# Performance work log

Measured on AMD Instinct MI355X. Metric: run time of the kernel, lower is better.

The kernel has to match this reference:

```python
import jax, jax.numpy as jnp
import numpy as np

B, T, P, V, D, DINO, H, L = 32, 40, 256, 4096, 256, 384, 4, 2
HD = D // H          # head dim 64
DFF = 4 * D          # 1024
EPS = 1e-5


def setup_inputs() -> dict:
    key = jax.random.key(0)
    ks = iter(jax.random.split(key, 40))
    rn = lambda shape, s=0.02: jax.random.normal(next(ks), shape, jnp.float32) * s
    return dict(
        patches=jax.random.normal(next(ks), (B, P, DINO), jnp.float32),
        tokens=jax.random.randint(next(ks), (B, T), 0, V, jnp.int32),
        tok_emb=rn((V, D)),
        pos_emb=rn((1, T, D)),
        qkv_w=rn((L, 3 * D, D)), qkv_b=jnp.zeros((L, 3 * D), jnp.float32),
        out_w=rn((L, D, D)), out_b=jnp.zeros((L, D), jnp.float32),
        ln1_s=jnp.ones((L, D), jnp.float32), ln1_b=jnp.zeros((L, D), jnp.float32),
        w1=rn((L, DFF, D)), b1=jnp.zeros((L, DFF), jnp.float32),
        w2=rn((L, D, DFF)), b2=jnp.zeros((L, D), jnp.float32),
        ln2_s=jnp.ones((L, D), jnp.float32), ln2_b=jnp.zeros((L, D), jnp.float32),
        fus_w1=rn((D, DINO + D)), fus_b1=jnp.zeros((D,), jnp.float32),
        fus_w2=rn((D, D)), fus_b2=jnp.zeros((D,), jnp.float32),
        cls_w=rn((V, D)), cls_b=jnp.zeros((V,), jnp.float32),
    )


def _ln(x, s, b):
    m = jnp.mean(x, -1, keepdims=True)
    v = jnp.var(x, -1, keepdims=True)
    return (x - m) * jax.lax.rsqrt(v + EPS) * s + b


def _token_encoder(tokens, tok_emb, pos_emb, qkv_w, qkv_b, out_w, out_b,
                   ln1_s, ln1_b, w1, b1, w2, b2, ln2_s, ln2_b):
    # Causal full-sequence pass: output at position t equals re-running the
    # unmasked encoder on tokens[:, :t+1] and taking the last position.
    x = tok_emb[tokens] + pos_emb[:, :tokens.shape[1], :]   # [B,T,D]
    causal = jnp.triu(jnp.full((T, T), -1e9, jnp.float32), 1)  # [T,T]
    for l in range(L):  # fixed small layer count
        qkv = x @ qkv_w[l].T + qkv_b[l]                     # [B,T,3D]
        q, k, v = jnp.split(qkv, 3, axis=-1)
        q = q.reshape(B, T, H, HD).transpose(0, 2, 1, 3)    # [B,H,T,hd]
        k = k.reshape(B, T, H, HD).transpose(0, 2, 1, 3)
        v = v.reshape(B, T, H, HD).transpose(0, 2, 1, 3)
        scores = jnp.einsum('bhqd,bhkd->bhqk', q, k) / np.sqrt(HD).astype(np.float32)
        attn = jax.nn.softmax(scores + causal, axis=-1)
        ctx = jnp.einsum('bhqk,bhkd->bhqd', attn, v)        # [B,H,T,hd]
        ctx = ctx.transpose(0, 2, 1, 3).reshape(B, T, D)
        x = _ln(x + ctx @ out_w[l].T + out_b[l], ln1_s[l], ln1_b[l])
        h = jax.nn.relu(x @ w1[l].T + b1[l]) @ w2[l].T + b2[l]
        x = _ln(x + h, ln2_s[l], ln2_b[l])
    return x  # [B,T,D]


def reference(patches, tokens, tok_emb, pos_emb, qkv_w, qkv_b, out_w, out_b,
              ln1_s, ln1_b, w1, b1, w2, b2, ln2_s, ln2_b,
              fus_w1, fus_b1, fus_w2, fus_b2, cls_w, cls_b):
    enc = _token_encoder(tokens, tok_emb, pos_emb, qkv_w, qkv_b, out_w, out_b,
                         ln1_s, ln1_b, w1, b1, w2, b2, ln2_s, ln2_b)  # [B,T,D]
    # context for step 0 is zeros; step t>0 uses encoder output at position t-1
    ctx = jnp.concatenate([jnp.zeros((B, 1, D), enc.dtype), enc[:, :-1]], axis=1)  # [B,T,D]
    # fusion MLP: split the concat-linear into a patch part and a context part
    wp, wc = fus_w1[:, :DINO], fus_w1[:, DINO:]
    pproj = patches @ wp.T                                  # [B,P,D]
    cproj = ctx @ wc.T + fus_b1                             # [B,T,D]
    h = jax.nn.gelu(pproj[:, None, :, :] + cproj[:, :, None, :], approximate=False)  # [B,T,P,D]
    fused = h @ fus_w2.T + fus_b2                           # [B,T,P,D]
    # sigmoid+gather of the 4096-way logits == gather classifier rows, dot, sigmoid
    w_sel = cls_w[tokens]                                   # [B,T,D]
    b_sel = cls_b[tokens]                                   # [B,T]
    logits = jnp.einsum('btpd,btd->btp', fused, w_sel) + b_sel[:, :, None]
    probs = jax.nn.sigmoid(logits)                          # [B,T,P]
    return probs.transpose(0, 2, 1)                         # [B,P,T] == [B,256,40]
```

## Files before the change

kernel.cpp:

```cpp
#include <hip/hip_runtime.h>
#include <hip/hip_bf16.h>

#define B_ 32
#define T_ 40
#define P_ 256
#define V_ 4096
#define D_ 256
#define DINO_ 384
#define H_ 4
#define L_ 2
#define HD_ 64
#define DFF_ 1024
#define EPS_ 1e-5f

typedef __bf16 bf16;
typedef __bf16 bf16x8 __attribute__((ext_vector_type(8)));
typedef float f32x4 __attribute__((ext_vector_type(4)));

#define FUS_ELEMS 163840
#define FUS_BLOCKS 80
#define PAT_BLOCKS 1536
#define PREP_UNITS 2960

__device__ __forceinline__ bf16x8 cvt8(const float* p) {
  float4 f0 = *(const float4*)p;
  float4 f1 = *(const float4*)(p + 4);
  bf16x8 v;
  v[0] = (bf16)f0.x; v[1] = (bf16)f0.y; v[2] = (bf16)f0.z; v[3] = (bf16)f0.w;
  v[4] = (bf16)f1.x; v[5] = (bf16)f1.y; v[6] = (bf16)f1.z; v[7] = (bf16)f1.w;
  return v;
}

struct GemmSM  { bf16 As[32 * 72];  bf16 Ws[32 * 72]; };
struct CprojSM { bf16 As[32 * 264]; bf16 Ws[32 * 72]; };
struct AttnSM  { float q[20][65]; float k[40][65]; float v[40][65]; float s[20][41]; };
struct PrepSM  { float tile[32][33]; };
struct FinalSM { float2 cws[4][D_]; };

struct Params {
  const float* patches; const int* tokens; const float* tok_emb; const float* pos_emb;
  const float* qkv_w; const float* qkv_b; const float* out_w; const float* out_b;
  const float* ln1_s; const float* ln1_b; const float* w1; const float* b1;
  const float* w2; const float* b2; const float* ln2_s; const float* ln2_b;
  const float* fus_w1; const float* fus_b1; const float* fus_w2; const float* fus_b2;
  const float* cls_w; const float* cls_b; float* out;
  float* x; float* qkvbuf; float* attbuf; float* s; float* pprojT; float* cw;
  bf16* wb; bf16* w2Tb; bf16* patb; bf16* hb;
};

template <int ABF16, int WF32, int OBF16, int RELU, int RESID, int GATH, int CW>
__device__ __forceinline__ void tile_gemm(
    bf16* As, bf16* Ws, const void* Av, const void* Wv, const float* bias,
    const float* resid, const int* tokens, void* outv, int K, int lda,
    int ldw, int ldc, int bm, int bn) {
  const int tid = threadIdx.x;
  const int lane = tid & 63;
  const int wv = tid >> 6;
  const int mi = wv & 1, ni = wv >> 1;
  const int col = lane & 15, quad = lane >> 4;
  const int srow = tid >> 3, kc = (tid & 7) * 8;
  const float* Af = (const float*)Av;
  const bf16* Ab = (const bf16*)Av;
  const float* Ag = GATH ? (Af + (long)tokens[bm + srow] * D_) : nullptr;
  const float* Wpf = (const float*)Wv + (long)(bn + srow) * ldw + kc;
  const bf16* Wpb = (const bf16*)Wv + (long)(bn + srow) * ldw + kc;

  f32x4 acc = {0.f, 0.f, 0.f, 0.f};
  for (int kk = 0; kk < K; kk += 64) {
    if (GATH)
      *(bf16x8*)&As[srow * 72 + kc] = cvt8(Ag + kk + kc);
    else if (ABF16)
      *(bf16x8*)&As[srow * 72 + kc] = *(const bf16x8*)(Ab + (long)(bm + srow) * lda + kk + kc);
    else
      *(bf16x8*)&As[srow * 72 + kc] = cvt8(Af + (long)(bm + srow) * lda + kk + kc);
    if (WF32)
      *(bf16x8*)&Ws[srow * 72 + kc] = cvt8(Wpf + kk);
    else
      *(bf16x8*)&Ws[srow * 72 + kc] = *(const bf16x8*)(Wpb + kk);
    __syncthreads();
#pragma unroll
    for (int ki = 0; ki < 2; ++ki) {
      bf16x8 afr = *(const bf16x8*)&As[(mi * 16 + col) * 72 + ki * 32 + quad * 8];
      bf16x8 bfr = *(const bf16x8*)&Ws[(ni * 16 + col) * 72 + ki * 32 + quad * 8];
      acc = __builtin_amdgcn_mfma_f32_16x16x32_bf16(afr, bfr, acc, 0, 0, 0);
    }
    __syncthreads();
  }
  const int n = bn + ni * 16 + col;
  float bv = bias ? bias[n] : 0.0f;
#pragma unroll
  for (int r = 0; r < 4; ++r) {
    int m = bm + mi * 16 + quad * 4 + r;
    float val = acc[r] + bv;
    if (RESID) val += resid[(long)m * D_ + n];
    if (RELU) val = fmaxf(val, 0.0f);
    if (CW == 1) ((float*)outv)[(long)m * (2 * D_) + n * 2] = val;
    else if (CW == 2) ((float*)outv)[(long)m * (2 * D_) + n * 2 + 1] = val;
    else if (OBF16) ((bf16*)outv)[(long)m * ldc + n] = (bf16)val;
    else ((float*)outv)[(long)m * ldc + n] = val;
  }
}

__device__ __forceinline__ void do_prep(PrepSM& ps, const Params& P, int u) {
  int tid = threadIdx.x;
  if (u < 1280) {
    P.x[u * D_ + tid] = P.tok_emb[(long)P.tokens[u] * D_ + tid] + P.pos_emb[(u % T_) * D_ + tid];
  } else if (u < 1344) {
    int tt = u - 1280;
    int bx = (tt & 7) * 32, by = (tt >> 3) * 32;
    int tx = tid & 31, ty = tid >> 5;
#pragma unroll
    for (int i = 0; i < 32; i += 8) ps.tile[ty + i][tx] = P.fus_w2[(by + ty + i) * D_ + bx + tx];
    __syncthreads();
#pragma unroll
    for (int i = 0; i < 32; i += 8)
      P.w2Tb[(bx + ty + i) * D_ + by + tx] = (bf16)ps.tile[tx][ty + i];
  } else if (u < 1344 + FUS_BLOCKS) {
    long f = (long)(u - 1344) * 2048 + tid * 8;
    *(bf16x8*)&P.wb[f] = cvt8(P.fus_w1 + f);
  } else {
    long f = (long)(u - 1344 - FUS_BLOCKS) * 2048 + tid * 8;
    *(bf16x8*)&P.patb[f] = cvt8(P.patches + f);
  }
}

__device__ __forceinline__ void do_qkv(GemmSM& g, const Params& P, int l, int u) {
  tile_gemm<0, 1, 0, 0, 0, 0, 0>(g.As, g.Ws, P.x, P.qkv_w + (long)l * 3 * D_ * D_,
                                 P.qkv_b + l * 3 * D_, nullptr, nullptr, P.qkvbuf,
                                 256, D_, D_, 3 * D_, (u / 24) * 32, (u % 24) * 32);
}
__device__ __forceinline__ void do_proj(GemmSM& g, const Params& P, int l, int u) {
  tile_gemm<0, 1, 0, 0, 1, 0, 0>(g.As, g.Ws, P.attbuf, P.out_w + (long)l * D_ * D_,
                                 P.out_b + l * D_, P.x, nullptr, P.s,
                                 256, D_, D_, D_, (u / 8) * 32, (u % 8) * 32);
}
__device__ __forceinline__ void do_w1(GemmSM& g, const Params& P, int l, int u) {
  tile_gemm<0, 1, 1, 1, 0, 0, 0>(g.As, g.Ws, P.x, P.w1 + (long)l * DFF_ * D_,
                                 P.b1 + l * DFF_, nullptr, nullptr, P.hb,
                                 256, D_, D_, DFF_, (u / 32) * 32, (u % 32) * 32);
}
__device__ __forceinline__ void do_w2(GemmSM& g, const Params& P, int l, int u) {
  tile_gemm<1, 1, 0, 0, 1, 0, 0>(g.As, g.Ws, P.hb, P.w2 + (long)l * D_ * DFF_,
                                 P.b2 + l * D_, P.x, nullptr, P.s,
                                 DFF_, DFF_, DFF_, D_, (u / 8) * 32, (u % 8) * 32);
}
__device__ __forceinline__ void do_pproj(GemmSM& g, const Params& P, int t) {
  int bn = (t & 7) * 32; int y = t >> 3; int bb = y >> 3; int bm = (y & 7) * 32;
  tile_gemm<1, 0, 0, 0, 0, 0, 0>(g.As, g.Ws, P.wb, P.patb + (long)bb * P_ * DINO_,
                                 nullptr, nullptr, nullptr, P.pprojT + (long)bb * D_ * P_,
                                 384, 640, DINO_, P_, bm, bn);
}
__device__ __forceinline__ void do_weff(GemmSM& g, const Params& P, int t) {
  tile_gemm<0, 0, 0, 0, 0, 1, 2>(g.As, g.Ws, P.cls_w, P.w2Tb, nullptr, nullptr,
                                 P.tokens, P.cw, 256, D_, D_, D_,
                                 (t / 8) * 32, (t % 8) * 32);
}

__device__ __forceinline__ void do_attn(AttnSM& A, const Params& P, int u) {
  int h = u & 3, b = (u >> 2) & 31, zq = u >> 7;
  int r0 = zq * 20;
  int tid = threadIdx.x;
  int lane = tid & 63, wv = tid >> 6;
  const float* qkv = P.qkvbuf;
  for (int idx = tid; idx < T_ * HD_; idx += 256) {
    int t = idx >> 6, d = idx & 63;
    long base = (long)(b * T_ + t) * (3 * D_) + h * HD_ + d;
    A.k[t][d] = qkv[base + D_];
    A.v[t][d] = qkv[base + 2 * D_];
    if (t < 20) A.q[t][d] = qkv[(long)(b * T_ + r0 + t) * (3 * D_) + h * HD_ + d];
  }
  __syncthreads();
  for (int idx = tid; idx < 20 * T_; idx += 256) {
    int i = idx / T_, j = idx - i * T_;
    if (j <= r0 + i) {
      float acc = 0.f;
#pragma unroll
      for (int d = 0; d < HD_; ++d) acc += A.q[i][d] * A.k[j][d];
      A.s[i][j] = acc * 0.125f;
    }
  }
  __syncthreads();
  for (int rr = wv; rr < 20; rr += 4) {
    int hi = r0 + rr;
    float val = (lane <= hi) ? A.s[rr][lane] : -1e30f;
    float mx = val;
#pragma unroll
    for (int mk = 1; mk < 64; mk <<= 1) mx = fmaxf(mx, __shfl_xor(mx, mk));
    float e = (lane <= hi)
                  ? __builtin_amdgcn_exp2f((val - mx) * 1.4426950408889634f)
                  : 0.f;
    float sum = e;
#pragma unroll
    for (int mk = 1; mk < 64; mk <<= 1) sum += __shfl_xor(sum, mk);
    float inv = __builtin_amdgcn_rcpf(sum);
    if (lane < T_) A.s[rr][lane] = e * inv;
  }
  __syncthreads();
  for (int idx = tid; idx < 20 * HD_; idx += 256) {
    int i = idx >> 6, d = idx & 63;
    int hi = r0 + i;
    float acc = 0.f;
    for (int j = 0; j <= hi; ++j) acc += A.s[i][j] * A.v[j][d];
    P.attbuf[(long)(b * T_ + hi) * D_ + h * HD_ + d] = acc;
  }
}

__device__ __forceinline__ void do_cproj(CprojSM& c, const Params& P, int bm, int bn) {
  const int tid = threadIdx.x;
  const int lane = tid & 63;
  const int wv = tid >> 6;
  const int mi = wv & 1, ni = wv >> 1;
  const int col = lane & 15, quad = lane >> 4;
  const int srow = tid >> 3, kc = (tid & 7) * 8;
  const int gm = bm + srow;
  f32x4 acc = {0.f, 0.f, 0.f, 0.f};
  const int cg = (tid & 7) * 32;
  const int t = gm % T_;
  if (t == 0) {
    bf16x8 z8 = {};
#pragma unroll
    for (int i = 0; i < 4; ++i) *(bf16x8*)&c.As[srow * 264 + cg + i * 8] = z8;
  } else {
    const float* sp = P.s + (long)(gm - 1) * D_ + cg;
    float v[32];
    float sum = 0.f, ss = 0.f;
#pragma unroll
    for (int i = 0; i < 8; ++i) {
      float4 f = *(const float4*)(sp + i * 4);
      v[i*4] = f.x; v[i*4+1] = f.y; v[i*4+2] = f.z; v[i*4+3] = f.w;
      sum += f.x + f.y + f.z + f.w;
      ss += f.x*f.x + f.y*f.y + f.z*f.z + f.w*f.w;
    }
#pragma unroll
    for (int mk = 1; mk < 8; mk <<= 1) {
      sum += __shfl_xor(sum, mk);
      ss += __shfl_xor(ss, mk);
    }
    float mean = sum * (1.0f / D_);
    float inv = rsqrtf(ss * (1.0f / D_) - mean * mean + EPS_);
    const float* lng = P.ln2_s + D_;
    const float* lnb = P.ln2_b + D_;
#pragma unroll
    for (int i = 0; i < 8; ++i) {
      float4 g4 = *(const float4*)(lng + cg + i * 4);
      float4 b4 = *(const float4*)(lnb + cg + i * 4);
      c.As[srow*264 + cg + i*4]     = (bf16)((v[i*4]   - mean) * inv * g4.x + b4.x);
      c.As[srow*264 + cg + i*4 + 1] = (bf16)((v[i*4+1] - mean) * inv * g4.y + b4.y);
      c.As[srow*264 + cg + i*4 + 2] = (bf16)((v[i*4+2] - mean) * inv * g4.z + b4.z);
      c.As[srow*264 + cg + i*4 + 3] = (bf16)((v[i*4+3] - mean) * inv * g4.w + b4.w);
    }
  }
  __syncthreads();
  const bf16* Wp = P.wb + 384 + (long)(bn + srow) * 640 + kc;
  for (int kk = 0; kk < 256; kk += 64) {
    *(bf16x8*)&c.Ws[srow * 72 + kc] = *(const bf16x8*)(Wp + kk);
    __syncthreads();
#pragma unroll
    for (int ki = 0; ki < 2; ++ki) {
      bf16x8 afr = *(const bf16x8*)&c.As[(mi*16 + col) * 264 + kk + ki*32 + quad*8];
      bf16x8 bfr = *(const bf16x8*)&c.Ws[(ni*16 + col) * 72 + ki*32 + quad*8];
      acc = __builtin_amdgcn_mfma_f32_16x16x32_bf16(afr, bfr, acc, 0, 0, 0);
    }
    __syncthreads();
  }
  const int n = bn + ni * 16 + col;
  float bv = P.fus_b1[n];
#pragma unroll
  for (int r = 0; r < 4; ++r) {
    int m = bm + mi * 16 + quad * 4 + r;
    P.cw[(long)m * (2 * D_) + n * 2] = acc[r] + bv;
  }
}

__device__ __forceinline__ void do_final(FinalSM& F, const Params& P, int u) {
  int tid = threadIdx.x;
  int lane = tid & 63, wv = tid >> 6;
  int px = u & 3, rest = u >> 2;
  int ty = rest % 10, b = rest / 10;
  int p = px * 64 + lane;
  int t = ty * 4 + wv;
  int mbase = b * T_ + ty * 4;
  for (int idx = tid; idx < 4 * D_; idx += 256) {
    int tt = idx >> 8, e = idx & 255;
    F.cws[tt][e] = ((const float2*)P.cw)[(long)(mbase + tt) * D_ + e];
  }
  __syncthreads();

  int m = b * T_ + t;
  int tok = P.tokens[m];
  const float* cr = P.cls_w + (long)tok * D_;
  float bacc = 0.f;
#pragma unroll
  for (int i = 0; i < 4; ++i) bacc += cr[lane + i * 64] * P.fus_b2[lane + i * 64];
#pragma unroll
  for (int mk = 1; mk < 64; mk <<= 1) bacc += __shfl_xor(bacc, mk);
  float beff = bacc + P.cls_b[tok];

  const float* ppb = P.pprojT + (long)b * (D_ * P_);
  float acc = 0.f;
#pragma unroll 8
  for (int e = 0; e < D_; ++e) {
    float pp = ppb[e * P_ + p];
    float2 c = F.cws[wv][e];
    float x = pp + c.x;
    float ex = __builtin_amdgcn_exp2f(-2.4554248f * x);
    float r = __builtin_amdgcn_rcpf(1.0f + ex);
    acc = fmaf(x * r, c.y, acc);
  }
  float logit = acc + beff;
  float es = __builtin_amdgcn_exp2f(-1.4426950408889634f * logit);
  P.out[(long)(b * P_ + p) * T_ + t] = __builtin_amdgcn_rcpf(1.0f + es);
}

__global__ __launch_bounds__(256) void prep_k(Params P) {
  __shared__ PrepSM ps; do_prep(ps, P, blockIdx.x);
}
__global__ __launch_bounds__(256) void qkv_k(Params P, int l) {
  __shared__ GemmSM g; do_qkv(g, P, l, blockIdx.x);
}
__global__ __launch_bounds__(256) void apw_k(Params P) {
  __shared__ union __align__(16) { AttnSM a; GemmSM g; } sm;
  int bid = blockIdx.x;
  if (bid < 256) do_attn(sm.a, P, bid);
  else if (bid < 2304) do_pproj(sm.g, P, bid - 256);
  else do_weff(sm.g, P, bid - 2304);
}
__global__ __launch_bounds__(256) void attn_k(Params P) {
  __shared__ AttnSM a; do_attn(a, P, blockIdx.x);
}
__global__ __launch_bounds__(256) void proj_k(Params P, int l) {
  __shared__ GemmSM g; do_proj(g, P, l, blockIdx.x);
}
__global__ __launch_bounds__(256) void ln_k(const float* __restrict__ s,
                                            float* __restrict__ xout,
                                            const float* __restrict__ g,
                                            const float* __restrict__ be) {
  int wv = threadIdx.x >> 6, lane = threadIdx.x & 63;
  int m = blockIdx.x * 4 + wv;
  float4 v = *(const float4*)(s + (long)m * D_ + lane * 4);
  float sum = v.x + v.y + v.z + v.w;
  float ss = v.x * v.x + v.y * v.y + v.z * v.z + v.w * v.w;
#pragma unroll
  for (int mk = 1; mk < 64; mk <<= 1) {
    sum += __shfl_xor(sum, mk);
    ss += __shfl_xor(ss, mk);
  }
  float mean = sum * (1.0f / D_);
  float inv = rsqrtf(ss * (1.0f / D_) - mean * mean + EPS_);
  float4 g4 = *(const float4*)(g + lane * 4);
  float4 b4 = *(const float4*)(be + lane * 4);
  float4 o;
  o.x = (v.x - mean) * inv * g4.x + b4.x;
  o.y = (v.y - mean) * inv * g4.y + b4.y;
  o.z = (v.z - mean) * inv * g4.z + b4.z;
  o.w = (v.w - mean) * inv * g4.w + b4.w;
  *(float4*)(xout + (long)m * D_ + lane * 4) = o;
}
__global__ __launch_bounds__(256) void w1_k(Params P, int l) {
  __shared__ GemmSM g; do_w1(g, P, l, blockIdx.x);
}
__global__ __launch_bounds__(256) void w2_k(Params P, int l) {
  __shared__ GemmSM g; do_w2(g, P, l, blockIdx.x);
}
__global__ __launch_bounds__(256) void cproj_k(Params P) {
  __shared__ CprojSM c; do_cproj(c, P, (blockIdx.x >> 3) * 32, (blockIdx.x & 7) * 32);
}
__global__ __launch_bounds__(256) void final_k(Params P) {
  __shared__ FinalSM f; do_final(f, P, blockIdx.x);
}

extern "C" void kernel_launch(void* const* d_in, const int* in_sizes, int n_in, void* d_out,
                              int out_size, void* d_ws, size_t ws_size, hipStream_t stream) {
  Params P;
  P.patches = (const float*)d_in[0];
  P.tokens = (const int*)d_in[1];
  P.tok_emb = (const float*)d_in[2];
  P.pos_emb = (const float*)d_in[3];
  P.qkv_w = (const float*)d_in[4];
  P.qkv_b = (const float*)d_in[5];
  P.out_w = (const float*)d_in[6];
  P.out_b = (const float*)d_in[7];
  P.ln1_s = (const float*)d_in[8];
  P.ln1_b = (const float*)d_in[9];
  P.w1 = (const float*)d_in[10];
  P.b1 = (const float*)d_in[11];
  P.w2 = (const float*)d_in[12];
  P.b2 = (const float*)d_in[13];
  P.ln2_s = (const float*)d_in[14];
  P.ln2_b = (const float*)d_in[15];
  P.fus_w1 = (const float*)d_in[16];
  P.fus_b1 = (const float*)d_in[17];
  P.fus_w2 = (const float*)d_in[18];
  P.fus_b2 = (const float*)d_in[19];
  P.cls_w = (const float*)d_in[20];
  P.cls_b = (const float*)d_in[21];
  P.out = (float*)d_out;

  const int MT = B_ * T_;
  P.x = (float*)d_ws;
  P.qkvbuf = P.x + MT * D_;
  P.attbuf = P.qkvbuf + MT * 3 * D_;
  P.s = P.attbuf + MT * D_;
  P.pprojT = P.s + MT * D_;
  P.cw = P.pprojT + (long)B_ * D_ * P_;
  P.wb = (bf16*)(P.cw + MT * D_ * 2);
  P.w2Tb = P.wb + FUS_ELEMS;
  P.patb = P.w2Tb + D_ * D_;
  P.hb = P.patb + (long)B_ * P_ * DINO_;

  prep_k<<<PREP_UNITS, 256, 0, stream>>>(P);
  qkv_k<<<960, 256, 0, stream>>>(P, 0);
  apw_k<<<2624, 256, 0, stream>>>(P);
  proj_k<<<320, 256, 0, stream>>>(P, 0);
  ln_k<<<320, 256, 0, stream>>>(P.s, P.x, P.ln1_s, P.ln1_b);
  w1_k<<<1280, 256, 0, stream>>>(P, 0);
  w2_k<<<320, 256, 0, stream>>>(P, 0);
  ln_k<<<320, 256, 0, stream>>>(P.s, P.x, P.ln2_s, P.ln2_b);
  qkv_k<<<960, 256, 0, stream>>>(P, 1);
  attn_k<<<256, 256, 0, stream>>>(P);
  proj_k<<<320, 256, 0, stream>>>(P, 1);
  ln_k<<<320, 256, 0, stream>>>(P.s, P.x, P.ln1_s + D_, P.ln1_b + D_);
  w1_k<<<1280, 256, 0, stream>>>(P, 1);
  w2_k<<<320, 256, 0, stream>>>(P, 1);
  cproj_k<<<320, 256, 0, stream>>>(P);
  final_k<<<1280, 256, 0, stream>>>(P);
}
```

Before: 249.6 us.

## Spread patch-projection and weff tiles across small encoder kernels; coarsen prep blocks

The 2048 independent patch-projection tiles, previously packed into one large kernel with attention, are split into four chunks of 512. Those chunks now ride along with the under-filled layer-0 QKV, attention, W2 and layer-1 QKV launches, and the weff work moves into the layer-0 output-projection launch. The intent is to fill idle compute units during the small encoder GEMMs and shorten the critical path. The prep kernel also gets coarser blocks: float4 embedding rows, four rows per block, and four conversion chunks per block. This cuts the launch from 2960 blocks to 788. The risk is load imbalance, since the heavier pproj tiles can now extend those kernels.

Measured after the change: 249.0 us. Within noise of the previous version (-0.2%).

```diff
diff --git a/kernel.cpp b/kernel.cpp
--- a/kernel.cpp
+++ b/kernel.cpp
@@ -18,9 +18,9 @@
 typedef float f32x4 __attribute__((ext_vector_type(4)));
 
 #define FUS_ELEMS 163840
-#define FUS_BLOCKS 80
-#define PAT_BLOCKS 1536
-#define PREP_UNITS 2960
+#define FUS_BLOCKS 20
+#define PAT_BLOCKS 384
+#define PREP_UNITS 788
 
 __device__ __forceinline__ bf16x8 cvt8(const float* p) {
   float4 f0 = *(const float4*)p;
@@ -103,10 +103,17 @@
 
 __device__ __forceinline__ void do_prep(PrepSM& ps, const Params& P, int u) {
   int tid = threadIdx.x;
-  if (u < 1280) {
-    P.x[u * D_ + tid] = P.tok_emb[(long)P.tokens[u] * D_ + tid] + P.pos_emb[(u % T_) * D_ + tid];
-  } else if (u < 1344) {
-    int tt = u - 1280;
+  if (u < 320) {
+    int r = tid >> 6, lane = tid & 63;
+    int m = u * 4 + r;
+    long eb = (long)P.tokens[m] * D_ + lane * 4;
+    long pb = (long)(m % T_) * D_ + lane * 4;
+    float4 e = *(const float4*)(P.tok_emb + eb);
+    float4 p = *(const float4*)(P.pos_emb + pb);
+    float4 o; o.x = e.x + p.x; o.y = e.y + p.y; o.z = e.z + p.z; o.w = e.w + p.w;
+    *(float4*)(P.x + (long)m * D_ + lane * 4) = o;
+  } else if (u < 384) {
+    int tt = u - 320;
     int bx = (tt & 7) * 32, by = (tt >> 3) * 32;
     int tx = tid & 31, ty = tid >> 5;
 #pragma unroll
@@ -115,12 +122,20 @@
 #pragma unroll
     for (int i = 0; i < 32; i += 8)
       P.w2Tb[(bx + ty + i) * D_ + by + tx] = (bf16)ps.tile[tx][ty + i];
-  } else if (u < 1344 + FUS_BLOCKS) {
-    long f = (long)(u - 1344) * 2048 + tid * 8;
-    *(bf16x8*)&P.wb[f] = cvt8(P.fus_w1 + f);
+  } else if (u < 384 + FUS_BLOCKS) {
+    long base = (long)(u - 384) * 8192;
+#pragma unroll
+    for (int j = 0; j < 4; ++j) {
+      long f = base + j * 2048 + tid * 8;
+      *(bf16x8*)&P.wb[f] = cvt8(P.fus_w1 + f);
+    }
   } else {
-    long f = (long)(u - 1344 - FUS_BLOCKS) * 2048 + tid * 8;
-    *(bf16x8*)&P.patb[f] = cvt8(P.patches + f);
+    long base = (long)(u - 384 - FUS_BLOCKS) * 8192;
+#pragma unroll
+    for (int j = 0; j < 4; ++j) {
+      long f = base + j * 2048 + tid * 8;
+      *(bf16x8*)&P.patb[f] = cvt8(P.patches + f);
+    }
   }
 }
 
@@ -315,18 +330,27 @@
 __global__ __launch_bounds__(256) void prep_k(Params P) {
   __shared__ PrepSM ps; do_prep(ps, P, blockIdx.x);
 }
-__global__ __launch_bounds__(256) void qkv_k(Params P, int l) {
-  __shared__ GemmSM g; do_qkv(g, P, l, blockIdx.x);
-}
-__global__ __launch_bounds__(256) void apw_k(Params P) {
+template <int L, int CH>
+__global__ __launch_bounds__(256) void qkvp_k(Params P) {
+  __shared__ GemmSM g;
+  int bid = blockIdx.x;
+  if (bid < 960) do_qkv(g, P, L, bid);
+  else do_pproj(g, P, bid - 960 + CH * 512);
+}
+__global__ __launch_bounds__(256) void attnp_k(Params P) {
   __shared__ union __align__(16) { AttnSM a; GemmSM g; } sm;
   int bid = blockIdx.x;
   if (bid < 256) do_attn(sm.a, P, bid);
-  else if (bid < 2304) do_pproj(sm.g, P, bid - 256);
-  else do_weff(sm.g, P, bid - 2304);
+  else do_pproj(sm.g, P, bid - 256 + 512);
 }
 __global__ __launch_bounds__(256) void attn_k(Params P) {
   __shared__ AttnSM a; do_attn(a, P, blockIdx.x);
+}
+__global__ __launch_bounds__(256) void projw_k(Params P) {
+  __shared__ GemmSM g;
+  int bid = blockIdx.x;
+  if (bid < 320) do_proj(g, P, 0, bid);
+  else do_weff(g, P, bid - 320);
 }
 __global__ __launch_bounds__(256) void proj_k(Params P, int l) {
   __shared__ GemmSM g; do_proj(g, P, l, blockIdx.x);
@@ -358,6 +382,12 @@
 }
 __global__ __launch_bounds__(256) void w1_k(Params P, int l) {
   __shared__ GemmSM g; do_w1(g, P, l, blockIdx.x);
+}
+__global__ __launch_bounds__(256) void w2p_k(Params P) {
+  __shared__ GemmSM g;
+  int bid = blockIdx.x;
+  if (bid < 320) do_w2(g, P, 0, bid);
+  else do_pproj(g, P, bid - 320 + 1024);
 }
 __global__ __launch_bounds__(256) void w2_k(Params P, int l) {
   __shared__ GemmSM g; do_w2(g, P, l, blockIdx.x);
@@ -409,14 +439,14 @@
   P.hb = P.patb + (long)B_ * P_ * DINO_;
 
   prep_k<<<PREP_UNITS, 256, 0, stream>>>(P);
-  qkv_k<<<960, 256, 0, stream>>>(P, 0);
-  apw_k<<<2624, 256, 0, stream>>>(P);
-  proj_k<<<320, 256, 0, stream>>>(P, 0);
+  qkvp_k<0, 0><<<1472, 256, 0, stream>>>(P);
+  attnp_k<<<768, 256, 0, stream>>>(P);
+  projw_k<<<640, 256, 0, stream>>>(P);
   ln_k<<<320, 256, 0, stream>>>(P.s, P.x, P.ln1_s, P.ln1_b);
   w1_k<<<1280, 256, 0, stream>>>(P, 0);
-  w2_k<<<320, 256, 0, stream>>>(P, 0);
+  w2p_k<<<832, 256, 0, stream>>>(P);
   ln_k<<<320, 256, 0, stream>>>(P.s, P.x, P.ln2_s, P.ln2_b);
-  qkv_k<<<960, 256, 0, stream>>>(P, 1);
+  qkvp_k<1, 3><<<1472, 256, 0, stream>>>(P);
   attn_k<<<256, 256, 0, stream>>>(P);
   proj_k<<<320, 256, 0, stream>>>(P, 1);
   ln_k<<<320, 256, 0, stream>>>(P.s, P.x, P.ln1_s + D_, P.ln1_b + D_);
```
